# Kernel optimization log

Hardware: AMD Instinct MI355X
Metric: run time of the kernel (lower is better)

The kernel has to match this reference:

```python
import jax, jax.numpy as jnp
import numpy as np


def setup_inputs() -> dict:
    key = jax.random.key(0)
    ks = jax.random.split(key, 5)
    B, T, S = 64, 128, 1024
    IN_DIM, OUT_DIM = 1024, 1024
    decoder_output = jax.random.normal(ks[0], (B, T, OUT_DIM), dtype=jnp.float32)
    encoder_outputs = jax.random.normal(ks[1], (B, S, IN_DIM), dtype=jnp.float32)
    encoder_padding_mask = jax.random.randint(ks[2], (B, S), 0, 2).astype(bool)
    # nn.Linear(output_dim, input_dim, bias=False): weight [input_dim, output_dim]
    W_attn = jax.random.normal(ks[3], (IN_DIM, OUT_DIM), dtype=jnp.float32) * (1.0 / np.sqrt(OUT_DIM))
    # nn.Linear(input_dim+output_dim, output_dim): weight [output_dim, input_dim+output_dim]
    W_out = jax.random.normal(ks[4], (OUT_DIM, IN_DIM + OUT_DIM), dtype=jnp.float32) * (1.0 / np.sqrt(IN_DIM + OUT_DIM))
    b_out = jnp.zeros((OUT_DIM,), dtype=jnp.float32)
    return {"decoder_output": decoder_output, "encoder_outputs": encoder_outputs,
            "encoder_padding_mask": encoder_padding_mask,
            "W_attn": W_attn, "W_out": W_out, "b_out": b_out}


def reference(decoder_output, encoder_outputs, encoder_padding_mask, W_attn, W_out, b_out):
    # general score: bmm(attn(query), key^T)
    q_proj = jnp.einsum('bto,io->bti', decoder_output, W_attn)          # [B,T,in_dim]
    scores = jnp.einsum('bti,bsi->bts', q_proj, encoder_outputs)        # [B,T,S]
    scores = jnp.where(encoder_padding_mask[:, None, :], -jnp.inf, scores)
    attn_weights = jax.nn.softmax(scores, axis=-1)                      # [B,T,S]
    context = jnp.einsum('bts,bsi->bti', attn_weights, encoder_outputs) # [B,T,in_dim]
    cat = jnp.concatenate([context, decoder_output], axis=-1)           # [B,T,in+out]
    attn_outputs = jnp.tanh(jnp.einsum('btc,oc->bto', cat, W_out) + b_out)
    return attn_outputs, attn_weights
```

## Files before the change

kernel.cpp:

```cpp
#include <hip/hip_runtime.h>
#include <math.h>


typedef __attribute__((ext_vector_type(8))) short short8;
typedef __attribute__((ext_vector_type(4))) float f32x4;
typedef __attribute__((ext_vector_type(4))) unsigned short u16x4;

__device__ __forceinline__ unsigned int fbits(float x) {
    union { float f; unsigned int u; } v; v.f = x; return v.u;
}
__device__ __forceinline__ float asfloat(unsigned int u) {
    union { unsigned int u; float f; } v; v.u = u; return v.f;
}
__device__ __forceinline__ float truncbf(float x) { return asfloat(fbits(x) & 0xffff0000u); }
__device__ __forceinline__ unsigned int pkhi(float X, float Y) {
    return __builtin_amdgcn_perm(fbits(Y), fbits(X), 0x07060302u);
}
__device__ __forceinline__ unsigned short f2bf(float x) {
    unsigned int u = fbits(x);
    u += 0x7fffu + ((u >> 16) & 1u);
    return (unsigned short)(u >> 16);
}
__device__ __forceinline__ void g2lds16(const void* g, void* l) {
    __builtin_amdgcn_global_load_lds(
        (const __attribute__((address_space(1))) void*)g,
        (__attribute__((address_space(3))) void*)l, 16, 0, 0);
}

__global__ __launch_bounds__(256) void split_rtz(
    const float* __restrict__ src, unsigned short* __restrict__ hi,
    unsigned short* __restrict__ lo)
{
    long long i = (long long)blockIdx.x * 256 + threadIdx.x;
    float4 x = *(const float4*)(src + i * 4);
    uint2 h, l;
    h.x = pkhi(x.x, x.y); h.y = pkhi(x.z, x.w);
    float l0 = x.x - truncbf(x.x), l1 = x.y - truncbf(x.y);
    float l2 = x.z - truncbf(x.z), l3 = x.w - truncbf(x.w);
    l.x = pkhi(l0, l1); l.y = pkhi(l2, l3);
    *(uint2*)(hi + i * 4) = h;
    *(uint2*)(lo + i * 4) = l;
}

__global__ __launch_bounds__(256) void cvt_f32(
    const float* __restrict__ src, unsigned short* __restrict__ dst)
{
    long long i = (long long)blockIdx.x * 256 + threadIdx.x;
    float4 x = *(const float4*)(src + i * 4);
    u16x4 h; h[0] = f2bf(x.x); h[1] = f2bf(x.y); h[2] = f2bf(x.z); h[3] = f2bf(x.w);
    *(u16x4*)(dst + i * 4) = h;
}

__global__ __launch_bounds__(256) void gemm3_qproj(
    const unsigned short* __restrict__ Ahi, const unsigned short* __restrict__ Alo,
    const unsigned short* __restrict__ Bhi, const unsigned short* __restrict__ Blo,
    unsigned short* __restrict__ Chi, unsigned short* __restrict__ Clo)
{
    const int m0 = blockIdx.x * 128, n0 = blockIdx.y * 128;
    __shared__ __align__(16) unsigned short Ah[128*32], Al[128*32], Bh[128*32], Bl[128*32];

    const int tid = threadIdx.x, lane = tid & 63, wave = tid >> 6;
    const int wm = (wave & 1) * 64, wn = (wave >> 1) * 64;
    const int fr = lane & 15, kq = lane >> 4;
    const int row0 = tid >> 2, c80 = (tid & 3) * 8;

    f32x4 zero = {0.f, 0.f, 0.f, 0.f};
    f32x4 acc[4][4];
    #pragma unroll
    for (int i = 0; i < 4; i++)
        #pragma unroll
        for (int j = 0; j < 4; j++) acc[i][j] = zero;

    for (int k0 = 0; k0 < 1024; k0 += 32) {
        const unsigned short* pa = Ahi + (long long)(m0 + row0) * 1024 + k0 + c80;
        const unsigned short* pl = Alo + (long long)(m0 + row0) * 1024 + k0 + c80;
        const unsigned short* pb = Bhi + (long long)(n0 + row0) * 1024 + k0 + c80;
        const unsigned short* pm = Blo + (long long)(n0 + row0) * 1024 + k0 + c80;
        g2lds16(pa,            &Ah[tid*8]);
        g2lds16(pa + 64*1024,  &Ah[tid*8 + 2048]);
        g2lds16(pl,            &Al[tid*8]);
        g2lds16(pl + 64*1024,  &Al[tid*8 + 2048]);
        g2lds16(pb,            &Bh[tid*8]);
        g2lds16(pb + 64*1024,  &Bh[tid*8 + 2048]);
        g2lds16(pm,            &Bl[tid*8]);
        g2lds16(pm + 64*1024,  &Bl[tid*8 + 2048]);
        __syncthreads();

        short8 fah[4], fal[4], fbh[4], fbl[4];
        #pragma unroll
        for (int fi = 0; fi < 4; fi++) {
            fah[fi] = *(const short8*)&Ah[(wm + fi*16 + fr)*32 + kq*8];
            fal[fi] = *(const short8*)&Al[(wm + fi*16 + fr)*32 + kq*8];
            fbh[fi] = *(const short8*)&Bh[(wn + fi*16 + fr)*32 + kq*8];
            fbl[fi] = *(const short8*)&Bl[(wn + fi*16 + fr)*32 + kq*8];
        }
        #pragma unroll
        for (int fi = 0; fi < 4; fi++)
            #pragma unroll
            for (int fj = 0; fj < 4; fj++) {
                acc[fi][fj] = __builtin_amdgcn_mfma_f32_16x16x32_bf16(fah[fi], fbh[fj], acc[fi][fj], 0, 0, 0);
                acc[fi][fj] = __builtin_amdgcn_mfma_f32_16x16x32_bf16(fah[fi], fbl[fj], acc[fi][fj], 0, 0, 0);
                acc[fi][fj] = __builtin_amdgcn_mfma_f32_16x16x32_bf16(fal[fi], fbh[fj], acc[fi][fj], 0, 0, 0);
            }
        __syncthreads();
    }

    #pragma unroll
    for (int fi = 0; fi < 4; fi++) {
        int rb = m0 + wm + fi*16 + kq*4;
        #pragma unroll
        for (int fj = 0; fj < 4; fj++) {
            int col = n0 + wn + fj*16 + fr;
            #pragma unroll
            for (int j = 0; j < 4; j++) {
                float x = acc[fi][fj][j];
                unsigned int hb = fbits(x) & 0xffff0000u;
                Chi[(long long)(rb + j) * 1024 + col] = (unsigned short)(hb >> 16);
                float l = x - asfloat(hb);
                Clo[(long long)(rb + j) * 1024 + col] = (unsigned short)(fbits(l) >> 16);
            }
        }
    }
}

__global__ __launch_bounds__(256) void gemm3_scores(
    const unsigned short* __restrict__ Qhi, const unsigned short* __restrict__ Qlo,
    const float* __restrict__ enc, float* __restrict__ C)
{
    const int bz = blockIdx.z, n0 = blockIdx.y * 128;
    const unsigned short* Ahb = Qhi + (long long)bz * 128 * 1024;
    const unsigned short* Alb = Qlo + (long long)bz * 128 * 1024;
    const float* Bb = enc + (long long)bz * 1024 * 1024;
    float* Cb = C + (long long)bz * 128 * 1024;

    __shared__ __align__(16) unsigned short Ah[128*32], Al[128*32], Bh[128*32], Bl[128*32];

    const int tid = threadIdx.x, lane = tid & 63, wave = tid >> 6;
    const int wm = (wave & 1) * 64, wn = (wave >> 1) * 64;
    const int fr = lane & 15, kq = lane >> 4;
    const int row0 = tid >> 2, c80 = (tid & 3) * 8;

    f32x4 zero = {0.f, 0.f, 0.f, 0.f};
    f32x4 acc[4][4];
    #pragma unroll
    for (int i = 0; i < 4; i++)
        #pragma unroll
        for (int j = 0; j < 4; j++) acc[i][j] = zero;

    for (int k0 = 0; k0 < 1024; k0 += 32) {
        const unsigned short* pa = Ahb + (long long)row0 * 1024 + k0 + c80;
        const unsigned short* pl = Alb + (long long)row0 * 1024 + k0 + c80;
        g2lds16(pa,           &Ah[tid*8]);
        g2lds16(pa + 64*1024, &Ah[tid*8 + 2048]);
        g2lds16(pl,           &Al[tid*8]);
        g2lds16(pl + 64*1024, &Al[tid*8 + 2048]);

        #pragma unroll
        for (int i = 0; i < 4; i++) {
            int u = i * 256 + tid;
            int row = u >> 3, c4 = (u & 7) * 4;
            float4 b4 = *(const float4*)(Bb + (long long)(n0 + row) * 1024 + k0 + c4);
            uint2 hh, ll;
            hh.x = pkhi(b4.x, b4.y); hh.y = pkhi(b4.z, b4.w);
            float l0 = b4.x - truncbf(b4.x), l1 = b4.y - truncbf(b4.y);
            float l2 = b4.z - truncbf(b4.z), l3 = b4.w - truncbf(b4.w);
            ll.x = pkhi(l0, l1); ll.y = pkhi(l2, l3);
            *(uint2*)&Bh[row*32 + c4] = hh;
            *(uint2*)&Bl[row*32 + c4] = ll;
        }
        __syncthreads();

        short8 fah[4], fal[4], fbh[4], fbl[4];
        #pragma unroll
        for (int fi = 0; fi < 4; fi++) {
            fah[fi] = *(const short8*)&Ah[(wm + fi*16 + fr)*32 + kq*8];
            fal[fi] = *(const short8*)&Al[(wm + fi*16 + fr)*32 + kq*8];
            fbh[fi] = *(const short8*)&Bh[(wn + fi*16 + fr)*32 + kq*8];
            fbl[fi] = *(const short8*)&Bl[(wn + fi*16 + fr)*32 + kq*8];
        }
        #pragma unroll
        for (int fi = 0; fi < 4; fi++)
            #pragma unroll
            for (int fj = 0; fj < 4; fj++) {
                acc[fi][fj] = __builtin_amdgcn_mfma_f32_16x16x32_bf16(fah[fi], fbh[fj], acc[fi][fj], 0, 0, 0);
                acc[fi][fj] = __builtin_amdgcn_mfma_f32_16x16x32_bf16(fah[fi], fbl[fj], acc[fi][fj], 0, 0, 0);
                acc[fi][fj] = __builtin_amdgcn_mfma_f32_16x16x32_bf16(fal[fi], fbh[fj], acc[fi][fj], 0, 0, 0);
            }
        __syncthreads();
    }

    #pragma unroll
    for (int fi = 0; fi < 4; fi++) {
        int rb = wm + fi*16 + kq*4;
        #pragma unroll
        for (int fj = 0; fj < 4; fj++) {
            int col = n0 + wn + fj*16 + fr;
            #pragma unroll
            for (int j = 0; j < 4; j++)
                Cb[(long long)(rb + j) * 1024 + col] = acc[fi][fj][j];
        }
    }
}

__global__ __launch_bounds__(256) void softmax_mask(
    float* __restrict__ sw, const int* __restrict__ mask,
    unsigned short* __restrict__ wbf)
{
    const int row = blockIdx.x;
    const int b = row >> 7;
    const int tid = threadIdx.x, lane = tid & 63, wave = tid >> 6;
    float* sr = sw + (long long)row * 1024;
    const int* mr = mask + (long long)b * 1024;

    float4 x = *(const float4*)(sr + tid * 4);
    int4  mk = *(const int4*)(mr + tid * 4);
    float v0 = mk.x ? -INFINITY : x.x;
    float v1 = mk.y ? -INFINITY : x.y;
    float v2 = mk.z ? -INFINITY : x.z;
    float v3 = mk.w ? -INFINITY : x.w;

    float mx = fmaxf(fmaxf(v0, v1), fmaxf(v2, v3));
    #pragma unroll
    for (int off = 32; off; off >>= 1) mx = fmaxf(mx, __shfl_xor(mx, off));
    __shared__ float redm[4], reds[4];
    if (lane == 0) redm[wave] = mx;
    __syncthreads();
    mx = fmaxf(fmaxf(redm[0], redm[1]), fmaxf(redm[2], redm[3]));

    float p0 = __expf(v0 - mx), p1 = __expf(v1 - mx);
    float p2 = __expf(v2 - mx), p3 = __expf(v3 - mx);
    float s = (p0 + p1) + (p2 + p3);
    #pragma unroll
    for (int off = 32; off; off >>= 1) s += __shfl_xor(s, off);
    if (lane == 0) reds[wave] = s;
    __syncthreads();
    s = (reds[0] + reds[1]) + (reds[2] + reds[3]);
    float inv = 1.0f / s;

    float w0 = p0*inv, w1 = p1*inv, w2 = p2*inv, w3 = p3*inv;
    float4 w4; w4.x = w0; w4.y = w1; w4.z = w2; w4.w = w3;
    *(float4*)(sr + tid * 4) = w4;
    u16x4 wb; wb[0] = f2bf(w0); wb[1] = f2bf(w1); wb[2] = f2bf(w2); wb[3] = f2bf(w3);
    *(u16x4*)(wbf + (long long)row * 1024 + tid * 4) = wb;
}

#define BSTR 40
__global__ __launch_bounds__(256) void gemm_ctx(
    const unsigned short* __restrict__ Wb, const float* __restrict__ enc,
    unsigned short* __restrict__ ctx)
{
    const int bz = blockIdx.z, n0 = blockIdx.y * 128;
    const unsigned short* Ab = Wb + (long long)bz * 128 * 1024;
    const float* Bb = enc + (long long)bz * 1024 * 1024;

    __shared__ __align__(16) unsigned short Ah[128*32];
    __shared__ __align__(16) unsigned short Bt[128*BSTR];

    const int tid = threadIdx.x, lane = tid & 63, wave = tid >> 6;
    const int wm = (wave & 1) * 64, wn = (wave >> 1) * 64;
    const int fr = lane & 15, kq = lane >> 4;
    const int row0 = tid >> 2, c80 = (tid & 3) * 8;
    const int kb = tid & 7, nb = tid >> 3;

    f32x4 zero = {0.f, 0.f, 0.f, 0.f};
    f32x4 acc[4][4];
    #pragma unroll
    for (int i = 0; i < 4; i++)
        #pragma unroll
        for (int j = 0; j < 4; j++) acc[i][j] = zero;

    for (int k0 = 0; k0 < 1024; k0 += 32) {
        const unsigned short* pa = Ab + (long long)row0 * 1024 + k0 + c80;
        g2lds16(pa,           &Ah[tid*8]);
        g2lds16(pa + 64*1024, &Ah[tid*8 + 2048]);

        float4 r0 = *(const float4*)(Bb + (long long)(k0 + kb*4 + 0) * 1024 + n0 + nb*4);
        float4 r1 = *(const float4*)(Bb + (long long)(k0 + kb*4 + 1) * 1024 + n0 + nb*4);
        float4 r2 = *(const float4*)(Bb + (long long)(k0 + kb*4 + 2) * 1024 + n0 + nb*4);
        float4 r3 = *(const float4*)(Bb + (long long)(k0 + kb*4 + 3) * 1024 + n0 + nb*4);
        uint2 c;
        c.x = pkhi(r0.x, r1.x); c.y = pkhi(r2.x, r3.x);
        *(uint2*)&Bt[(nb*4 + 0)*BSTR + kb*4] = c;
        c.x = pkhi(r0.y, r1.y); c.y = pkhi(r2.y, r3.y);
        *(uint2*)&Bt[(nb*4 + 1)*BSTR + kb*4] = c;
        c.x = pkhi(r0.z, r1.z); c.y = pkhi(r2.z, r3.z);
        *(uint2*)&Bt[(nb*4 + 2)*BSTR + kb*4] = c;
        c.x = pkhi(r0.w, r1.w); c.y = pkhi(r2.w, r3.w);
        *(uint2*)&Bt[(nb*4 + 3)*BSTR + kb*4] = c;
        __syncthreads();

        short8 fa[4], fb[4];
        #pragma unroll
        for (int fi = 0; fi < 4; fi++) {
            fa[fi] = *(const short8*)&Ah[(wm + fi*16 + fr)*32 + kq*8];
            fb[fi] = *(const short8*)&Bt[(wn + fi*16 + fr)*BSTR + kq*8];
        }
        #pragma unroll
        for (int fi = 0; fi < 4; fi++)
            #pragma unroll
            for (int fj = 0; fj < 4; fj++)
                acc[fi][fj] = __builtin_amdgcn_mfma_f32_16x16x32_bf16(fa[fi], fb[fj], acc[fi][fj], 0, 0, 0);
        __syncthreads();
    }

    #pragma unroll
    for (int fi = 0; fi < 4; fi++) {
        int rb = bz * 128 + wm + fi*16 + kq*4;
        #pragma unroll
        for (int fj = 0; fj < 4; fj++) {
            int col = n0 + wn + fj*16 + fr;
            #pragma unroll
            for (int j = 0; j < 4; j++)
                ctx[(long long)(rb + j) * 1024 + col] = f2bf(acc[fi][fj][j]);
        }
    }
}

__global__ __launch_bounds__(256) void gemm_out(
    const unsigned short* __restrict__ ctx, const unsigned short* __restrict__ dech,
    const unsigned short* __restrict__ Wb, const float* __restrict__ bias,
    float* __restrict__ out)
{
    const int m0 = blockIdx.x * 128, n0 = blockIdx.y * 128;
    __shared__ __align__(16) unsigned short Ah[128*32], Bh[128*32];

    const int tid = threadIdx.x, lane = tid & 63, wave = tid >> 6;
    const int wm = (wave & 1) * 64, wn = (wave >> 1) * 64;
    const int fr = lane & 15, kq = lane >> 4;
    const int row0 = tid >> 2, c80 = (tid & 3) * 8;

    f32x4 zero = {0.f, 0.f, 0.f, 0.f};
    f32x4 acc[4][4];
    #pragma unroll
    for (int i = 0; i < 4; i++)
        #pragma unroll
        for (int j = 0; j < 4; j++) acc[i][j] = zero;

    for (int k0 = 0; k0 < 2048; k0 += 32) {
        const unsigned short* As = (k0 < 1024) ? ctx : dech;
        int kk = k0 & 1023;
        const unsigned short* pa = As + (long long)(m0 + row0) * 1024 + kk + c80;
        const unsigned short* pb = Wb + (long long)(n0 + row0) * 2048 + k0 + c80;
        g2lds16(pa,           &Ah[tid*8]);
        g2lds16(pa + 64*1024, &Ah[tid*8 + 2048]);
        g2lds16(pb,           &Bh[tid*8]);
        g2lds16(pb + 64*2048, &Bh[tid*8 + 2048]);
        __syncthreads();

        short8 fa[4], fb[4];
        #pragma unroll
        for (int fi = 0; fi < 4; fi++) {
            fa[fi] = *(const short8*)&Ah[(wm + fi*16 + fr)*32 + kq*8];
            fb[fi] = *(const short8*)&Bh[(wn + fi*16 + fr)*32 + kq*8];
        }
        #pragma unroll
        for (int fi = 0; fi < 4; fi++)
            #pragma unroll
            for (int fj = 0; fj < 4; fj++)
                acc[fi][fj] = __builtin_amdgcn_mfma_f32_16x16x32_bf16(fa[fi], fb[fj], acc[fi][fj], 0, 0, 0);
        __syncthreads();
    }

    #pragma unroll
    for (int fi = 0; fi < 4; fi++) {
        int rb = m0 + wm + fi*16 + kq*4;
        #pragma unroll
        for (int fj = 0; fj < 4; fj++) {
            int col = n0 + wn + fj*16 + fr;
            float bb = bias[col];
            #pragma unroll
            for (int j = 0; j < 4; j++)
                out[(long long)(rb + j) * 1024 + col] = tanhf(acc[fi][fj][j] + bb);
        }
    }
}

extern "C" void kernel_launch(void* const* d_in, const int* in_sizes, int n_in,
                              void* d_out, int out_size, void* d_ws, size_t ws_size,
                              hipStream_t stream) {
    const float* dec    = (const float*)d_in[0];
    const float* enc    = (const float*)d_in[1];
    const int*   mask   = (const int*)d_in[2];
    const float* W_attn = (const float*)d_in[3];
    const float* W_out  = (const float*)d_in[4];
    const float* b_out  = (const float*)d_in[5];

    float* out_attn = (float*)d_out;
    float* weights  = out_attn + 8388608;

    char* ws = (char*)d_ws;
    unsigned short* dec_hi = (unsigned short*)(ws);
    unsigned short* dec_lo = (unsigned short*)(ws + (16 << 20));
    unsigned short* wa_hi  = (unsigned short*)(ws + (32 << 20));
    unsigned short* wa_lo  = (unsigned short*)(ws + (34 << 20));
    unsigned short* wout_b = (unsigned short*)(ws + (36 << 20));
    unsigned short* q_hi   = (unsigned short*)(ws + (40 << 20));
    unsigned short* q_lo   = (unsigned short*)(ws + (56 << 20));
    unsigned short* w_bf   = (unsigned short*)(ws + (72 << 20));
    unsigned short* ctx_bf = (unsigned short*)(ws + (88 << 20));

    dim3 blk(256);

    split_rtz<<<dim3(8192), blk, 0, stream>>>(dec, dec_hi, dec_lo);
    split_rtz<<<dim3(1024), blk, 0, stream>>>(W_attn, wa_hi, wa_lo);
    cvt_f32<<<dim3(2048), blk, 0, stream>>>(W_out, wout_b);

    gemm3_qproj<<<dim3(64, 8, 1), blk, 0, stream>>>(dec_hi, dec_lo, wa_hi, wa_lo, q_hi, q_lo);
    gemm3_scores<<<dim3(1, 8, 64), blk, 0, stream>>>(q_hi, q_lo, enc, weights);
    softmax_mask<<<dim3(8192), blk, 0, stream>>>(weights, mask, w_bf);
    gemm_ctx<<<dim3(1, 8, 64), blk, 0, stream>>>(w_bf, enc, ctx_bf);
    gemm_out<<<dim3(64, 8, 1), blk, 0, stream>>>(ctx_bf, dec_hi, wout_b, b_out, out_attn);
}
```

Measured before the change: 643.7 us.

## Use 8-wave blocks with 64x32 warp tiles across all four GEMM kernels

Each GEMM kernel now launches 512 threads (8 waves) per 128x128 tile instead of 256, so every wave computes a 64x32 sub-tile with half the accumulators. Each thread issues half as many global-to-LDS loads per k-step, which raises the number of waves per CU available to hide latency while keeping the tile size. The scores kernel also pads its B-operand LDS rows to a stride of 40 to reduce bank conflicts. In exchange, the A fragments are now read from LDS by twice as many waves, adding LDS traffic per MFMA.

Result: no change. 656.2 us (+1.9%).

```diff
diff --git a/kernel.cpp b/kernel.cpp
--- a/kernel.cpp
+++ b/kernel.cpp
@@ -51,7 +51,7 @@
     *(u16x4*)(dst + i * 4) = h;
 }
 
-__global__ __launch_bounds__(256) void gemm3_qproj(
+__global__ __launch_bounds__(512, 4) void gemm3_qproj(
     const unsigned short* __restrict__ Ahi, const unsigned short* __restrict__ Alo,
     const unsigned short* __restrict__ Bhi, const unsigned short* __restrict__ Blo,
     unsigned short* __restrict__ Chi, unsigned short* __restrict__ Clo)
@@ -60,44 +60,43 @@
     __shared__ __align__(16) unsigned short Ah[128*32], Al[128*32], Bh[128*32], Bl[128*32];
 
     const int tid = threadIdx.x, lane = tid & 63, wave = tid >> 6;
-    const int wm = (wave & 1) * 64, wn = (wave >> 1) * 64;
+    const int wm = (wave >> 2) * 64, wn = (wave & 3) * 32;
     const int fr = lane & 15, kq = lane >> 4;
     const int row0 = tid >> 2, c80 = (tid & 3) * 8;
 
     f32x4 zero = {0.f, 0.f, 0.f, 0.f};
-    f32x4 acc[4][4];
+    f32x4 acc[4][2];
     #pragma unroll
     for (int i = 0; i < 4; i++)
         #pragma unroll
-        for (int j = 0; j < 4; j++) acc[i][j] = zero;
+        for (int j = 0; j < 2; j++) acc[i][j] = zero;
 
     for (int k0 = 0; k0 < 1024; k0 += 32) {
         const unsigned short* pa = Ahi + (long long)(m0 + row0) * 1024 + k0 + c80;
         const unsigned short* pl = Alo + (long long)(m0 + row0) * 1024 + k0 + c80;
         const unsigned short* pb = Bhi + (long long)(n0 + row0) * 1024 + k0 + c80;
         const unsigned short* pm = Blo + (long long)(n0 + row0) * 1024 + k0 + c80;
-        g2lds16(pa,            &Ah[tid*8]);
-        g2lds16(pa + 64*1024,  &Ah[tid*8 + 2048]);
-        g2lds16(pl,            &Al[tid*8]);
-        g2lds16(pl + 64*1024,  &Al[tid*8 + 2048]);
-        g2lds16(pb,            &Bh[tid*8]);
-        g2lds16(pb + 64*1024,  &Bh[tid*8 + 2048]);
-        g2lds16(pm,            &Bl[tid*8]);
-        g2lds16(pm + 64*1024,  &Bl[tid*8 + 2048]);
-        __syncthreads();
-
-        short8 fah[4], fal[4], fbh[4], fbl[4];
+        g2lds16(pa, &Ah[tid*8]);
+        g2lds16(pl, &Al[tid*8]);
+        g2lds16(pb, &Bh[tid*8]);
+        g2lds16(pm, &Bl[tid*8]);
+        __syncthreads();
+
+        short8 fah[4], fal[4], fbh[2], fbl[2];
         #pragma unroll
         for (int fi = 0; fi < 4; fi++) {
             fah[fi] = *(const short8*)&Ah[(wm + fi*16 + fr)*32 + kq*8];
             fal[fi] = *(const short8*)&Al[(wm + fi*16 + fr)*32 + kq*8];
-            fbh[fi] = *(const short8*)&Bh[(wn + fi*16 + fr)*32 + kq*8];
-            fbl[fi] = *(const short8*)&Bl[(wn + fi*16 + fr)*32 + kq*8];
-        }
-        #pragma unroll
-        for (int fi = 0; fi < 4; fi++)
-            #pragma unroll
-            for (int fj = 0; fj < 4; fj++) {
+        }
+        #pragma unroll
+        for (int fj = 0; fj < 2; fj++) {
+            fbh[fj] = *(const short8*)&Bh[(wn + fj*16 + fr)*32 + kq*8];
+            fbl[fj] = *(const short8*)&Bl[(wn + fj*16 + fr)*32 + kq*8];
+        }
+        #pragma unroll
+        for (int fi = 0; fi < 4; fi++)
+            #pragma unroll
+            for (int fj = 0; fj < 2; fj++) {
                 acc[fi][fj] = __builtin_amdgcn_mfma_f32_16x16x32_bf16(fah[fi], fbh[fj], acc[fi][fj], 0, 0, 0);
                 acc[fi][fj] = __builtin_amdgcn_mfma_f32_16x16x32_bf16(fah[fi], fbl[fj], acc[fi][fj], 0, 0, 0);
                 acc[fi][fj] = __builtin_amdgcn_mfma_f32_16x16x32_bf16(fal[fi], fbh[fj], acc[fi][fj], 0, 0, 0);
@@ -109,7 +108,7 @@
     for (int fi = 0; fi < 4; fi++) {
         int rb = m0 + wm + fi*16 + kq*4;
         #pragma unroll
-        for (int fj = 0; fj < 4; fj++) {
+        for (int fj = 0; fj < 2; fj++) {
             int col = n0 + wn + fj*16 + fr;
             #pragma unroll
             for (int j = 0; j < 4; j++) {
@@ -123,7 +122,8 @@
     }
 }
 
-__global__ __launch_bounds__(256) void gemm3_scores(
+#define SSTR 40
+__global__ __launch_bounds__(512, 4) void gemm3_scores(
     const unsigned short* __restrict__ Qhi, const unsigned short* __restrict__ Qlo,
     const float* __restrict__ enc, float* __restrict__ C)
 {
@@ -133,31 +133,29 @@
     const float* Bb = enc + (long long)bz * 1024 * 1024;
     float* Cb = C + (long long)bz * 128 * 1024;
 
-    __shared__ __align__(16) unsigned short Ah[128*32], Al[128*32], Bh[128*32], Bl[128*32];
+    __shared__ __align__(16) unsigned short Ah[128*32], Al[128*32], Bh[128*SSTR], Bl[128*SSTR];
 
     const int tid = threadIdx.x, lane = tid & 63, wave = tid >> 6;
-    const int wm = (wave & 1) * 64, wn = (wave >> 1) * 64;
+    const int wm = (wave >> 2) * 64, wn = (wave & 3) * 32;
     const int fr = lane & 15, kq = lane >> 4;
     const int row0 = tid >> 2, c80 = (tid & 3) * 8;
 
     f32x4 zero = {0.f, 0.f, 0.f, 0.f};
-    f32x4 acc[4][4];
+    f32x4 acc[4][2];
     #pragma unroll
     for (int i = 0; i < 4; i++)
         #pragma unroll
-        for (int j = 0; j < 4; j++) acc[i][j] = zero;
+        for (int j = 0; j < 2; j++) acc[i][j] = zero;
 
     for (int k0 = 0; k0 < 1024; k0 += 32) {
         const unsigned short* pa = Ahb + (long long)row0 * 1024 + k0 + c80;
         const unsigned short* pl = Alb + (long long)row0 * 1024 + k0 + c80;
-        g2lds16(pa,           &Ah[tid*8]);
-        g2lds16(pa + 64*1024, &Ah[tid*8 + 2048]);
-        g2lds16(pl,           &Al[tid*8]);
-        g2lds16(pl + 64*1024, &Al[tid*8 + 2048]);
-
-        #pragma unroll
-        for (int i = 0; i < 4; i++) {
-            int u = i * 256 + tid;
+        g2lds16(pa, &Ah[tid*8]);
+        g2lds16(pl, &Al[tid*8]);
+
+        #pragma unroll
+        for (int i = 0; i < 2; i++) {
+            int u = i * 512 + tid;
             int row = u >> 3, c4 = (u & 7) * 4;
             float4 b4 = *(const float4*)(Bb + (long long)(n0 + row) * 1024 + k0 + c4);
             uint2 hh, ll;
@@ -165,23 +163,26 @@
             float l0 = b4.x - truncbf(b4.x), l1 = b4.y - truncbf(b4.y);
             float l2 = b4.z - truncbf(b4.z), l3 = b4.w - truncbf(b4.w);
             ll.x = pkhi(l0, l1); ll.y = pkhi(l2, l3);
-            *(uint2*)&Bh[row*32 + c4] = hh;
-            *(uint2*)&Bl[row*32 + c4] = ll;
-        }
-        __syncthreads();
-
-        short8 fah[4], fal[4], fbh[4], fbl[4];
+            *(uint2*)&Bh[row*SSTR + c4] = hh;
+            *(uint2*)&Bl[row*SSTR + c4] = ll;
+        }
+        __syncthreads();
+
+        short8 fah[4], fal[4], fbh[2], fbl[2];
         #pragma unroll
         for (int fi = 0; fi < 4; fi++) {
             fah[fi] = *(const short8*)&Ah[(wm + fi*16 + fr)*32 + kq*8];
             fal[fi] = *(const short8*)&Al[(wm + fi*16 + fr)*32 + kq*8];
-            fbh[fi] = *(const short8*)&Bh[(wn + fi*16 + fr)*32 + kq*8];
-            fbl[fi] = *(const short8*)&Bl[(wn + fi*16 + fr)*32 + kq*8];
-        }
-        #pragma unroll
-        for (int fi = 0; fi < 4; fi++)
-            #pragma unroll
-            for (int fj = 0; fj < 4; fj++) {
+        }
+        #pragma unroll
+        for (int fj = 0; fj < 2; fj++) {
+            fbh[fj] = *(const short8*)&Bh[(wn + fj*16 + fr)*SSTR + kq*8];
+            fbl[fj] = *(const short8*)&Bl[(wn + fj*16 + fr)*SSTR + kq*8];
+        }
+        #pragma unroll
+        for (int fi = 0; fi < 4; fi++)
+            #pragma unroll
+            for (int fj = 0; fj < 2; fj++) {
                 acc[fi][fj] = __builtin_amdgcn_mfma_f32_16x16x32_bf16(fah[fi], fbh[fj], acc[fi][fj], 0, 0, 0);
                 acc[fi][fj] = __builtin_amdgcn_mfma_f32_16x16x32_bf16(fah[fi], fbl[fj], acc[fi][fj], 0, 0, 0);
                 acc[fi][fj] = __builtin_amdgcn_mfma_f32_16x16x32_bf16(fal[fi], fbh[fj], acc[fi][fj], 0, 0, 0);
@@ -193,7 +194,7 @@
     for (int fi = 0; fi < 4; fi++) {
         int rb = wm + fi*16 + kq*4;
         #pragma unroll
-        for (int fj = 0; fj < 4; fj++) {
+        for (int fj = 0; fj < 2; fj++) {
             int col = n0 + wn + fj*16 + fr;
             #pragma unroll
             for (int j = 0; j < 4; j++)
@@ -245,7 +246,7 @@
 }
 
 #define BSTR 40
-__global__ __launch_bounds__(256) void gemm_ctx(
+__global__ __launch_bounds__(512, 4) void gemm_ctx(
     const unsigned short* __restrict__ Wb, const float* __restrict__ enc,
     unsigned short* __restrict__ ctx)
 {
@@ -257,48 +258,44 @@
     __shared__ __align__(16) unsigned short Bt[128*BSTR];
 
     const int tid = threadIdx.x, lane = tid & 63, wave = tid >> 6;
-    const int wm = (wave & 1) * 64, wn = (wave >> 1) * 64;
+    const int wm = (wave >> 2) * 64, wn = (wave & 3) * 32;
     const int fr = lane & 15, kq = lane >> 4;
     const int row0 = tid >> 2, c80 = (tid & 3) * 8;
-    const int kb = tid & 7, nb = tid >> 3;
+    const int kb = tid & 7, nb2 = tid >> 3;
 
     f32x4 zero = {0.f, 0.f, 0.f, 0.f};
-    f32x4 acc[4][4];
+    f32x4 acc[4][2];
     #pragma unroll
     for (int i = 0; i < 4; i++)
         #pragma unroll
-        for (int j = 0; j < 4; j++) acc[i][j] = zero;
+        for (int j = 0; j < 2; j++) acc[i][j] = zero;
 
     for (int k0 = 0; k0 < 1024; k0 += 32) {
         const unsigned short* pa = Ab + (long long)row0 * 1024 + k0 + c80;
-        g2lds16(pa,           &Ah[tid*8]);
-        g2lds16(pa + 64*1024, &Ah[tid*8 + 2048]);
-
-        float4 r0 = *(const float4*)(Bb + (long long)(k0 + kb*4 + 0) * 1024 + n0 + nb*4);
-        float4 r1 = *(const float4*)(Bb + (long long)(k0 + kb*4 + 1) * 1024 + n0 + nb*4);
-        float4 r2 = *(const float4*)(Bb + (long long)(k0 + kb*4 + 2) * 1024 + n0 + nb*4);
-        float4 r3 = *(const float4*)(Bb + (long long)(k0 + kb*4 + 3) * 1024 + n0 + nb*4);
-        uint2 c;
-        c.x = pkhi(r0.x, r1.x); c.y = pkhi(r2.x, r3.x);
-        *(uint2*)&Bt[(nb*4 + 0)*BSTR + kb*4] = c;
-        c.x = pkhi(r0.y, r1.y); c.y = pkhi(r2.y, r3.y);
-        *(uint2*)&Bt[(nb*4 + 1)*BSTR + kb*4] = c;
-        c.x = pkhi(r0.z, r1.z); c.y = pkhi(r2.z, r3.z);
-        *(uint2*)&Bt[(nb*4 + 2)*BSTR + kb*4] = c;
-        c.x = pkhi(r0.w, r1.w); c.y = pkhi(r2.w, r3.w);
-        *(uint2*)&Bt[(nb*4 + 3)*BSTR + kb*4] = c;
-        __syncthreads();
-
-        short8 fa[4], fb[4];
-        #pragma unroll
-        for (int fi = 0; fi < 4; fi++) {
+        g2lds16(pa, &Ah[tid*8]);
+
+        float2 r0 = *(const float2*)(Bb + (long long)(k0 + kb*4 + 0) * 1024 + n0 + nb2*2);
+        float2 r1 = *(const float2*)(Bb + (long long)(k0 + kb*4 + 1) * 1024 + n0 + nb2*2);
+        float2 r2 = *(const float2*)(Bb + (long long)(k0 + kb*4 + 2) * 1024 + n0 + nb2*2);
+        float2 r3 = *(const float2*)(Bb + (long long)(k0 + kb*4 + 3) * 1024 + n0 + nb2*2);
+        uint2 cc;
+        cc.x = pkhi(r0.x, r1.x); cc.y = pkhi(r2.x, r3.x);
+        *(uint2*)&Bt[(nb2*2 + 0)*BSTR + kb*4] = cc;
+        cc.x = pkhi(r0.y, r1.y); cc.y = pkhi(r2.y, r3.y);
+        *(uint2*)&Bt[(nb2*2 + 1)*BSTR + kb*4] = cc;
+        __syncthreads();
+
+        short8 fa[4], fb[2];
+        #pragma unroll
+        for (int fi = 0; fi < 4; fi++)
             fa[fi] = *(const short8*)&Ah[(wm + fi*16 + fr)*32 + kq*8];
-            fb[fi] = *(const short8*)&Bt[(wn + fi*16 + fr)*BSTR + kq*8];
-        }
-        #pragma unroll
-        for (int fi = 0; fi < 4; fi++)
-            #pragma unroll
-            for (int fj = 0; fj < 4; fj++)
+        #pragma unroll
+        for (int fj = 0; fj < 2; fj++)
+            fb[fj] = *(const short8*)&Bt[(wn + fj*16 + fr)*BSTR + kq*8];
+        #pragma unroll
+        for (int fi = 0; fi < 4; fi++)
+            #pragma unroll
+            for (int fj = 0; fj < 2; fj++)
                 acc[fi][fj] = __builtin_amdgcn_mfma_f32_16x16x32_bf16(fa[fi], fb[fj], acc[fi][fj], 0, 0, 0);
         __syncthreads();
     }
@@ -307,7 +304,7 @@
     for (int fi = 0; fi < 4; fi++) {
         int rb = bz * 128 + wm + fi*16 + kq*4;
         #pragma unroll
-        for (int fj = 0; fj < 4; fj++) {
+        for (int fj = 0; fj < 2; fj++) {
             int col = n0 + wn + fj*16 + fr;
             #pragma unroll
             for (int j = 0; j < 4; j++)
@@ -316,7 +313,7 @@
     }
 }
 
-__global__ __launch_bounds__(256) void gemm_out(
+__global__ __launch_bounds__(512, 4) void gemm_out(
     const unsigned short* __restrict__ ctx, const unsigned short* __restrict__ dech,
     const unsigned short* __restrict__ Wb, const float* __restrict__ bias,
     float* __restrict__ out)
@@ -325,38 +322,37 @@
     __shared__ __align__(16) unsigned short Ah[128*32], Bh[128*32];
 
     const int tid = threadIdx.x, lane = tid & 63, wave = tid >> 6;
-    const int wm = (wave & 1) * 64, wn = (wave >> 1) * 64;
+    const int wm = (wave >> 2) * 64, wn = (wave & 3) * 32;
     const int fr = lane & 15, kq = lane >> 4;
     const int row0 = tid >> 2, c80 = (tid & 3) * 8;
 
     f32x4 zero = {0.f, 0.f, 0.f, 0.f};
-    f32x4 acc[4][4];
+    f32x4 acc[4][2];
     #pragma unroll
     for (int i = 0; i < 4; i++)
         #pragma unroll
-        for (int j = 0; j < 4; j++) acc[i][j] = zero;
+        for (int j = 0; j < 2; j++) acc[i][j] = zero;
 
     for (int k0 = 0; k0 < 2048; k0 += 32) {
         const unsigned short* As = (k0 < 1024) ? ctx : dech;
         int kk = k0 & 1023;
         const unsigned short* pa = As + (long long)(m0 + row0) * 1024 + kk + c80;
         const unsigned short* pb = Wb + (long long)(n0 + row0) * 2048 + k0 + c80;
-        g2lds16(pa,           &Ah[tid*8]);
-        g2lds16(pa + 64*1024, &Ah[tid*8 + 2048]);
-        g2lds16(pb,           &Bh[tid*8]);
-        g2lds16(pb + 64*2048, &Bh[tid*8 + 2048]);
-        __syncthreads();
-
-        short8 fa[4], fb[4];
-        #pragma unroll
-        for (int fi = 0; fi < 4; fi++) {
+        g2lds16(pa, &Ah[tid*8]);
+        g2lds16(pb, &Bh[tid*8]);
+        __syncthreads();
+
+        short8 fa[4], fb[2];
+        #pragma unroll
+        for (int fi = 0; fi < 4; fi++)
             fa[fi] = *(const short8*)&Ah[(wm + fi*16 + fr)*32 + kq*8];
-            fb[fi] = *(const short8*)&Bh[(wn + fi*16 + fr)*32 + kq*8];
-        }
-        #pragma unroll
-        for (int fi = 0; fi < 4; fi++)
-            #pragma unroll
-            for (int fj = 0; fj < 4; fj++)
+        #pragma unroll
+        for (int fj = 0; fj < 2; fj++)
+            fb[fj] = *(const short8*)&Bh[(wn + fj*16 + fr)*32 + kq*8];
+        #pragma unroll
+        for (int fi = 0; fi < 4; fi++)
+            #pragma unroll
+            for (int fj = 0; fj < 2; fj++)
                 acc[fi][fj] = __builtin_amdgcn_mfma_f32_16x16x32_bf16(fa[fi], fb[fj], acc[fi][fj], 0, 0, 0);
         __syncthreads();
     }
@@ -365,7 +361,7 @@
     for (int fi = 0; fi < 4; fi++) {
         int rb = m0 + wm + fi*16 + kq*4;
         #pragma unroll
-        for (int fj = 0; fj < 4; fj++) {
+        for (int fj = 0; fj < 2; fj++) {
             int col = n0 + wn + fj*16 + fr;
             float bb = bias[col];
             #pragma unroll
@@ -399,15 +395,15 @@
     unsigned short* w_bf   = (unsigned short*)(ws + (72 << 20));
     unsigned short* ctx_bf = (unsigned short*)(ws + (88 << 20));
 
-    dim3 blk(256);
+    dim3 blk(256), blk8(512);
 
     split_rtz<<<dim3(8192), blk, 0, stream>>>(dec, dec_hi, dec_lo);
     split_rtz<<<dim3(1024), blk, 0, stream>>>(W_attn, wa_hi, wa_lo);
     cvt_f32<<<dim3(2048), blk, 0, stream>>>(W_out, wout_b);
 
-    gemm3_qproj<<<dim3(64, 8, 1), blk, 0, stream>>>(dec_hi, dec_lo, wa_hi, wa_lo, q_hi, q_lo);
-    gemm3_scores<<<dim3(1, 8, 64), blk, 0, stream>>>(q_hi, q_lo, enc, weights);
+    gemm3_qproj<<<dim3(64, 8, 1), blk8, 0, stream>>>(dec_hi, dec_lo, wa_hi, wa_lo, q_hi, q_lo);
+    gemm3_scores<<<dim3(1, 8, 64), blk8, 0, stream>>>(q_hi, q_lo, enc, weights);
     softmax_mask<<<dim3(8192), blk, 0, stream>>>(weights, mask, w_bf);
-    gemm_ctx<<<dim3(1, 8, 64), blk, 0, stream>>>(w_bf, enc, ctx_bf);
-    gemm_out<<<dim3(64, 8, 1), blk, 0, stream>>>(ctx_bf, dec_hi, wout_b, b_out, out_attn);
-}
+    gemm_ctx<<<dim3(1, 8, 64), blk8, 0, stream>>>(w_bf, enc, ctx_bf);
+    gemm_out<<<dim3(64, 8, 1), blk8, 0, stream>>>(ctx_bf, dec_hi, wout_b, b_out, out_attn);
+}
```

## Emit transposed bf16 encoder copy in scores kernel for direct ctx loads

Applied to the files above, without the earlier changes.

The scores GEMM now also writes a transposed, truncated-bf16 copy of the encoder outputs into a workspace buffer while it stages the encoder tile. The context GEMM then reads that buffer with direct global-to-LDS loads instead of loading fp32 rows and transposing and packing them in registers. This removes the fp32 read and the in-kernel transpose from the context GEMM. In exchange, the scores kernel gains 128 MB of scattered 2-byte stores at a large stride, and the workspace must be big enough for a region that starts at 104 MB.

New measurement: 663.3 us. 3.0% more time.

```diff
diff --git a/kernel.cpp b/kernel.cpp
--- a/kernel.cpp
+++ b/kernel.cpp
@@ -125,13 +125,15 @@
 
 __global__ __launch_bounds__(256) void gemm3_scores(
     const unsigned short* __restrict__ Qhi, const unsigned short* __restrict__ Qlo,
-    const float* __restrict__ enc, float* __restrict__ C)
+    const float* __restrict__ enc, float* __restrict__ C,
+    unsigned short* __restrict__ encT)
 {
     const int bz = blockIdx.z, n0 = blockIdx.y * 128;
     const unsigned short* Ahb = Qhi + (long long)bz * 128 * 1024;
     const unsigned short* Alb = Qlo + (long long)bz * 128 * 1024;
     const float* Bb = enc + (long long)bz * 1024 * 1024;
     float* Cb = C + (long long)bz * 128 * 1024;
+    unsigned short* Tb = encT + (long long)bz * 1024 * 1024;
 
     __shared__ __align__(16) unsigned short Ah[128*32], Al[128*32], Bh[128*32], Bl[128*32];
 
@@ -167,6 +169,11 @@
             ll.x = pkhi(l0, l1); ll.y = pkhi(l2, l3);
             *(uint2*)&Bh[row*32 + c4] = hh;
             *(uint2*)&Bl[row*32 + c4] = ll;
+            unsigned short* et = Tb + (long long)(k0 + c4) * 1024 + (n0 + row);
+            et[0]    = (unsigned short)(fbits(b4.x) >> 16);
+            et[1024] = (unsigned short)(fbits(b4.y) >> 16);
+            et[2048] = (unsigned short)(fbits(b4.z) >> 16);
+            et[3072] = (unsigned short)(fbits(b4.w) >> 16);
         }
         __syncthreads();
 
@@ -244,23 +251,20 @@
     *(u16x4*)(wbf + (long long)row * 1024 + tid * 4) = wb;
 }
 
-#define BSTR 40
 __global__ __launch_bounds__(256) void gemm_ctx(
-    const unsigned short* __restrict__ Wb, const float* __restrict__ enc,
+    const unsigned short* __restrict__ Wb, const unsigned short* __restrict__ encT,
     unsigned short* __restrict__ ctx)
 {
     const int bz = blockIdx.z, n0 = blockIdx.y * 128;
     const unsigned short* Ab = Wb + (long long)bz * 128 * 1024;
-    const float* Bb = enc + (long long)bz * 1024 * 1024;
-
-    __shared__ __align__(16) unsigned short Ah[128*32];
-    __shared__ __align__(16) unsigned short Bt[128*BSTR];
+    const unsigned short* Bb = encT + (long long)bz * 1024 * 1024;
+
+    __shared__ __align__(16) unsigned short Ah[128*32], Bt[128*32];
 
     const int tid = threadIdx.x, lane = tid & 63, wave = tid >> 6;
     const int wm = (wave & 1) * 64, wn = (wave >> 1) * 64;
     const int fr = lane & 15, kq = lane >> 4;
     const int row0 = tid >> 2, c80 = (tid & 3) * 8;
-    const int kb = tid & 7, nb = tid >> 3;
 
     f32x4 zero = {0.f, 0.f, 0.f, 0.f};
     f32x4 acc[4][4];
@@ -271,29 +275,18 @@
 
     for (int k0 = 0; k0 < 1024; k0 += 32) {
         const unsigned short* pa = Ab + (long long)row0 * 1024 + k0 + c80;
+        const unsigned short* pb = Bb + (long long)(n0 + row0) * 1024 + k0 + c80;
         g2lds16(pa,           &Ah[tid*8]);
         g2lds16(pa + 64*1024, &Ah[tid*8 + 2048]);
-
-        float4 r0 = *(const float4*)(Bb + (long long)(k0 + kb*4 + 0) * 1024 + n0 + nb*4);
-        float4 r1 = *(const float4*)(Bb + (long long)(k0 + kb*4 + 1) * 1024 + n0 + nb*4);
-        float4 r2 = *(const float4*)(Bb + (long long)(k0 + kb*4 + 2) * 1024 + n0 + nb*4);
-        float4 r3 = *(const float4*)(Bb + (long long)(k0 + kb*4 + 3) * 1024 + n0 + nb*4);
-        uint2 c;
-        c.x = pkhi(r0.x, r1.x); c.y = pkhi(r2.x, r3.x);
-        *(uint2*)&Bt[(nb*4 + 0)*BSTR + kb*4] = c;
-        c.x = pkhi(r0.y, r1.y); c.y = pkhi(r2.y, r3.y);
-        *(uint2*)&Bt[(nb*4 + 1)*BSTR + kb*4] = c;
-        c.x = pkhi(r0.z, r1.z); c.y = pkhi(r2.z, r3.z);
-        *(uint2*)&Bt[(nb*4 + 2)*BSTR + kb*4] = c;
-        c.x = pkhi(r0.w, r1.w); c.y = pkhi(r2.w, r3.w);
-        *(uint2*)&Bt[(nb*4 + 3)*BSTR + kb*4] = c;
+        g2lds16(pb,           &Bt[tid*8]);
+        g2lds16(pb + 64*1024, &Bt[tid*8 + 2048]);
         __syncthreads();
 
         short8 fa[4], fb[4];
         #pragma unroll
         for (int fi = 0; fi < 4; fi++) {
             fa[fi] = *(const short8*)&Ah[(wm + fi*16 + fr)*32 + kq*8];
-            fb[fi] = *(const short8*)&Bt[(wn + fi*16 + fr)*BSTR + kq*8];
+            fb[fi] = *(const short8*)&Bt[(wn + fi*16 + fr)*32 + kq*8];
         }
         #pragma unroll
         for (int fi = 0; fi < 4; fi++)
@@ -398,6 +391,7 @@
     unsigned short* q_lo   = (unsigned short*)(ws + (56 << 20));
     unsigned short* w_bf   = (unsigned short*)(ws + (72 << 20));
     unsigned short* ctx_bf = (unsigned short*)(ws + (88 << 20));
+    unsigned short* enc_t  = (unsigned short*)(ws + (104 << 20));
 
     dim3 blk(256);
 
@@ -406,8 +400,8 @@
     cvt_f32<<<dim3(2048), blk, 0, stream>>>(W_out, wout_b);
 
     gemm3_qproj<<<dim3(64, 8, 1), blk, 0, stream>>>(dec_hi, dec_lo, wa_hi, wa_lo, q_hi, q_lo);
-    gemm3_scores<<<dim3(1, 8, 64), blk, 0, stream>>>(q_hi, q_lo, enc, weights);
+    gemm3_scores<<<dim3(1, 8, 64), blk, 0, stream>>>(q_hi, q_lo, enc, weights, enc_t);
     softmax_mask<<<dim3(8192), blk, 0, stream>>>(weights, mask, w_bf);
-    gemm_ctx<<<dim3(1, 8, 64), blk, 0, stream>>>(w_bf, enc, ctx_bf);
+    gemm_ctx<<<dim3(1, 8, 64), blk, 0, stream>>>(w_bf, enc_t, ctx_bf);
     gemm_out<<<dim3(64, 8, 1), blk, 0, stream>>>(ctx_bf, dec_hi, wout_b, b_out, out_attn);
 }
```
